# Optimization experiments

Measured on AMD Instinct MI355X. Metric: run time of the kernel, lower is better.

## Reference

```python
import jax, jax.numpy as jnp
import numpy as np

N, E, D, H, ED = 50000, 800000, 64, 8, 16
DH = D // H  # 8


def setup_inputs() -> dict:
    key = jax.random.key(0)
    ks = jax.random.split(key, 16)
    s = 0.05
    return {
        "x": jax.random.normal(ks[0], (N, D), jnp.float32),
        "edge_index": jax.random.randint(ks[1], (2, E), 0, N, jnp.int32),
        "edge_attr": jax.random.normal(ks[2], (E, ED), jnp.float32),
        "Wq": jax.random.normal(ks[3], (D, D), jnp.float32) * s,
        "bq": jnp.zeros((D,), jnp.float32),
        "Wk": jax.random.normal(ks[4], (D, D), jnp.float32) * s,
        "bk": jnp.zeros((D,), jnp.float32),
        "Wv": jax.random.normal(ks[5], (D, D), jnp.float32) * s,
        "bv": jnp.zeros((D,), jnp.float32),
        "We": jax.random.normal(ks[6], (ED, D), jnp.float32) * s,
        "be": jnp.zeros((D,), jnp.float32),
        "Wskip": jax.random.normal(ks[7], (D, D), jnp.float32) * s,
        "bskip": jnp.zeros((D,), jnp.float32),
        "Wbeta": jax.random.normal(ks[8], (3 * D, 1), jnp.float32) * s,
        "gamma": jnp.ones((D,), jnp.float32),
        "beta_bn": jnp.zeros((D,), jnp.float32),
    }


def reference(x, edge_index, edge_attr, Wq, bq, Wk, bk, Wv, bv, We, be,
              Wskip, bskip, Wbeta, gamma, beta_bn):
    n, d = x.shape
    src, dst = edge_index[0], edge_index[1]
    # per-node projections, then gather per edge (PyG TransformerConv)
    q = (x @ Wq + bq).reshape(n, H, DH)
    k = (x @ Wk + bk).reshape(n, H, DH)
    v = (x @ Wv + bv).reshape(n, H, DH)
    e = (edge_attr @ We + be).reshape(-1, H, DH)
    ke = k[src] + e                      # [E,H,DH]
    ve = v[src] + e                      # [E,H,DH]
    logits = (q[dst] * ke).sum(-1) / jnp.sqrt(jnp.float32(DH))  # [E,H]
    # segment softmax over incoming edges of each destination node
    m = jax.ops.segment_max(logits, dst, num_segments=n)
    p = jnp.exp(logits - m[dst])
    denom = jax.ops.segment_sum(p, dst, num_segments=n)
    alpha = p / (denom[dst] + 1e-16)     # [E,H]
    out = jax.ops.segment_sum(alpha[:, :, None] * ve, dst, num_segments=n)
    out = out.reshape(n, d)              # concat heads
    # beta-gated skip connection (beta=True, root_weight=True)
    x_r = x @ Wskip + bskip
    g = jax.nn.sigmoid(jnp.concatenate([out, x_r, out - x_r], axis=-1) @ Wbeta)
    out = g * x_r + (1.0 - g) * out
    # BatchNorm1d (training forward: batch statistics), eps=1e-5
    mean = out.mean(axis=0)
    var = out.var(axis=0)
    out = (out - mean) * jax.lax.rsqrt(var + 1e-5) * gamma + beta_bn
    # LeakyReLU(0.01); dropout is identity in eval
    return jnp.where(out >= 0, out, 0.01 * out)
```

## Files before the change

kernel.cpp:

```cpp
#include <hip/hip_runtime.h>

#define D   64
#define H   8
#define DH  8
#define ED  16
#define QK_SCALE 0.35355339059327373f

typedef unsigned int uint_t;

__device__ __forceinline__ void fma4(float4& a, float s, const float4& w) {
    a.x += s * w.x; a.y += s * w.y; a.z += s * w.z; a.w += s * w.w;
}
__device__ __forceinline__ uint_t f2bf(float f) {
    uint_t u = __float_as_uint(f);
    return (u + 0x7FFFu + ((u >> 16) & 1u)) >> 16;
}
__device__ __forceinline__ float bf_lo(uint_t u) { return __uint_as_float(u << 16); }
__device__ __forceinline__ float bf_hi(uint_t u) { return __uint_as_float(u & 0xFFFF0000u); }

__global__ __launch_bounds__(256) void proj_qs_hist(
    const float* __restrict__ x,
    const float* __restrict__ Wq, const float* __restrict__ bq,
    const float* __restrict__ Ws, const float* __restrict__ bs,
    const float* __restrict__ We, const float* __restrict__ be,
    float* __restrict__ q, float* __restrict__ xr,
    uint_t* __restrict__ Ap, float* __restrict__ qbe, int N,
    const int* __restrict__ ei, int* __restrict__ cnt, int E, int projBlocks)
{
    __shared__ float sW[2][D * D];
    __shared__ float sWe[ED * D];
    __shared__ float sbe[D];
    if (blockIdx.x >= projBlocks) {
        int gid = (blockIdx.x - projBlocks) * 256 + threadIdx.x;
        if (gid < E) atomicAdd(&cnt[ei[E + gid]], 1);
        return;
    }
    {
        for (int t = threadIdx.x; t < D * D; t += 256) {
            sW[0][t] = Wq[t];
            sW[1][t] = Ws[t];
        }
        for (int t = threadIdx.x; t < ED * D; t += 256) sWe[t] = We[t];
        if (threadIdx.x < D) sbe[threadIdx.x] = be[threadIdx.x];
    }
    __syncthreads();

    int cg = (threadIdx.x & 15) * 4;
    float4 vbq = *(const float4*)(bq + cg);
    float4 vbs = *(const float4*)(bs + cg);
    int h  = cg >> 3;
    int hh = (cg >> 2) & 1;

    #pragma unroll 1
    for (int it = 0; it < 4; ++it) {
        int node = blockIdx.x * 64 + it * 16 + (threadIdx.x >> 4);
        if (node >= N) return;

        float4 aq = {0,0,0,0}, as_ = {0,0,0,0};
        const float* xrow = x + (size_t)node * D;

        #pragma unroll
        for (int i = 0; i < D; i += 4) {
            float4 xv = *(const float4*)(xrow + i);
            #pragma unroll
            for (int s = 0; s < 4; ++s) {
                float xs = (&xv.x)[s];
                fma4(aq,  xs, *(const float4*)(&sW[0][(i + s) * D + cg]));
                fma4(as_, xs, *(const float4*)(&sW[1][(i + s) * D + cg]));
            }
        }
        aq.x = (aq.x + vbq.x) * QK_SCALE;
        aq.y = (aq.y + vbq.y) * QK_SCALE;
        aq.z = (aq.z + vbq.z) * QK_SCALE;
        aq.w = (aq.w + vbq.w) * QK_SCALE;
        as_.x += vbs.x; as_.y += vbs.y; as_.z += vbs.z; as_.w += vbs.w;

        size_t o = (size_t)node * D + cg;
        *(float4*)(q  + o) = aq;
        *(float4*)(xr + o) = as_;

        float part[ED];
        #pragma unroll
        for (int i = 0; i < ED; ++i) {
            float pi = 0.f;
            #pragma unroll
            for (int s = 0; s < 4; ++s)
                pi += (&aq.x)[s] * sWe[i * D + cg + s];
            part[i] = pi;
        }
        float qb = 0.f;
        #pragma unroll
        for (int s = 0; s < 4; ++s) qb += (&aq.x)[s] * sbe[cg + s];
        #pragma unroll
        for (int i = 0; i < ED; ++i) part[i] += __shfl_xor(part[i], 1);
        qb += __shfl_xor(qb, 1);

        uint4 apk;
        apk.x = f2bf(part[hh * 8 + 0]) | (f2bf(part[hh * 8 + 1]) << 16);
        apk.y = f2bf(part[hh * 8 + 2]) | (f2bf(part[hh * 8 + 3]) << 16);
        apk.z = f2bf(part[hh * 8 + 4]) | (f2bf(part[hh * 8 + 5]) << 16);
        apk.w = f2bf(part[hh * 8 + 6]) | (f2bf(part[hh * 8 + 7]) << 16);
        *(uint4*)(Ap + (size_t)node * 64 + h * 8 + hh * 4) = apk;
        if (hh == 0) qbe[(size_t)node * 8 + h] = qb;
    }
}

__global__ __launch_bounds__(256) void proj_kv_scana(
    const float* __restrict__ x,
    const float* __restrict__ Wk, const float* __restrict__ bk,
    const float* __restrict__ Wv, const float* __restrict__ bv,
    uint_t* __restrict__ kvp, int N, int kvBlocks,
    const int* __restrict__ cnt, int* __restrict__ bsum)
{
    __shared__ float sW[2][D * D];
    __shared__ int red[256];
    if (blockIdx.x >= kvBlocks) {
        int t = threadIdx.x;
        int i = (blockIdx.x - kvBlocks) * 256 + t;
        red[t] = (i < N) ? cnt[i] : 0;
        __syncthreads();
        for (int s = 128; s > 0; s >>= 1) {
            if (t < s) red[t] += red[t + s];
            __syncthreads();
        }
        if (t == 0) bsum[blockIdx.x - kvBlocks] = red[0];
        return;
    }
    for (int t = threadIdx.x; t < D * D; t += 256) {
        sW[0][t] = Wk[t];
        sW[1][t] = Wv[t];
    }
    __syncthreads();

    int cg = (threadIdx.x & 15) * 4;
    float4 vbk = *(const float4*)(bk + cg);
    float4 vbv = *(const float4*)(bv + cg);

    #pragma unroll 1
    for (int it = 0; it < 4; ++it) {
        int node = blockIdx.x * 64 + it * 16 + (threadIdx.x >> 4);
        if (node >= N) return;

        float4 ak = {0,0,0,0}, av = {0,0,0,0};
        const float* xrow = x + (size_t)node * D;

        #pragma unroll
        for (int i = 0; i < D; i += 4) {
            float4 xv = *(const float4*)(xrow + i);
            #pragma unroll
            for (int s = 0; s < 4; ++s) {
                float xs = (&xv.x)[s];
                fma4(ak, xs, *(const float4*)(&sW[0][(i + s) * D + cg]));
                fma4(av, xs, *(const float4*)(&sW[1][(i + s) * D + cg]));
            }
        }
        ak.x += vbk.x; ak.y += vbk.y; ak.z += vbk.z; ak.w += vbk.w;
        av.x += vbv.x; av.y += vbv.y; av.z += vbv.z; av.w += vbv.w;

        uint4 pkv;
        pkv.x = f2bf(ak.x) | (f2bf(av.x) << 16);
        pkv.y = f2bf(ak.y) | (f2bf(av.y) << 16);
        pkv.z = f2bf(ak.z) | (f2bf(av.z) << 16);
        pkv.w = f2bf(ak.w) | (f2bf(av.w) << 16);
        *(uint4*)(kvp + (size_t)node * D + cg) = pkv;
    }
}

__global__ __launch_bounds__(256) void scan_b(int* __restrict__ bsum, int nb)
{
    __shared__ int sh[256];
    int t = threadIdx.x;
    int v = (t < nb) ? bsum[t] : 0;
    sh[t] = v;
    __syncthreads();
    for (int s = 1; s < 256; s <<= 1) {
        int a = (t >= s) ? sh[t - s] : 0;
        __syncthreads();
        sh[t] += a;
        __syncthreads();
    }
    if (t < nb) bsum[t] = sh[t] - v;
}

__global__ __launch_bounds__(256) void scan_c(
    const int* __restrict__ cnt, const int* __restrict__ bsum,
    int* __restrict__ row_start, int* __restrict__ cursor, int N, int E)
{
    __shared__ int sh[256];
    int t = threadIdx.x;
    int i = blockIdx.x * 256 + t;
    int v = (i < N) ? cnt[i] : 0;
    sh[t] = v;
    __syncthreads();
    for (int s = 1; s < 256; s <<= 1) {
        int a = (t >= s) ? sh[t - s] : 0;
        __syncthreads();
        sh[t] += a;
        __syncthreads();
    }
    int excl = sh[t] - v + bsum[blockIdx.x];
    if (i < N) { row_start[i] = excl; cursor[i] = excl; }
    if (i == N - 1) row_start[N] = E;
}

__global__ __launch_bounds__(256) void csr_scatter(
    const int* __restrict__ ei, const float4* __restrict__ ea4,
    int* __restrict__ cursor, int* __restrict__ srcs_s,
    uint_t* __restrict__ ea_s, int E)
{
    int gid = blockIdx.x * 256 + threadIdx.x;
    if (gid >= E) return;
    int src = ei[gid];
    int dst = ei[E + gid];
    float4 r0 = ea4[(size_t)gid * 4 + 0];
    float4 r1 = ea4[(size_t)gid * 4 + 1];
    float4 r2 = ea4[(size_t)gid * 4 + 2];
    float4 r3 = ea4[(size_t)gid * 4 + 3];
    int pos = atomicAdd(&cursor[dst], 1);
    srcs_s[pos] = src;
    uint4 p0, p1;
    p0.x = f2bf(r0.x) | (f2bf(r0.y) << 16);
    p0.y = f2bf(r0.z) | (f2bf(r0.w) << 16);
    p0.z = f2bf(r1.x) | (f2bf(r1.y) << 16);
    p0.w = f2bf(r1.z) | (f2bf(r1.w) << 16);
    p1.x = f2bf(r2.x) | (f2bf(r2.y) << 16);
    p1.y = f2bf(r2.z) | (f2bf(r2.w) << 16);
    p1.z = f2bf(r3.x) | (f2bf(r3.y) << 16);
    p1.w = f2bf(r3.z) | (f2bf(r3.w) << 16);
    *(uint4*)(ea_s + (size_t)pos * 8)     = p0;
    *(uint4*)(ea_s + (size_t)pos * 8 + 4) = p1;
}

__global__ __launch_bounds__(256, 4) void node_gather(
    const int*   __restrict__ row_start,
    const int*   __restrict__ srcs_s,
    const uint_t* __restrict__ ea_s,
    const float* __restrict__ We, const float* __restrict__ be,
    const float* __restrict__ q, const uint_t* __restrict__ kvp,
    const float* __restrict__ xr,
    const uint_t* __restrict__ Ap, const float* __restrict__ qbe,
    const float* __restrict__ Wbeta,
    float* __restrict__ out, float* __restrict__ S1p, float* __restrict__ S2p,
    int N)
{
    __shared__ float l1[4][D];
    __shared__ float l2[4][D];
    int lane = threadIdx.x & 63;
    int w    = threadIdx.x >> 6;
    int h    = lane & 7;
    int e    = lane >> 3;
    int cmix = h * 8 + e;
    int perm = (h << 3) | e;

    float rWe[ED];
    #pragma unroll
    for (int i = 0; i < ED; ++i) rWe[i] = We[i * D + cmix];
    float bev = be[cmix];
    float wb0 = Wbeta[lane], wb1 = Wbeta[D + lane], wb2 = Wbeta[2 * D + lane];

    float s1bn = 0.f, s2bn = 0.f;
    int stride = gridDim.x * 4;

    for (int nid = blockIdx.x * 4 + w; nid < N; nid += stride) {
        int rs  = row_start[nid];
        int deg = row_start[nid + 1] - rs;

        const float* qp = q + (size_t)nid * D + h * 8;
        float4 q0 = *(const float4*)qp;
        float4 q1 = *(const float4*)(qp + 4);
        const uint4* app = (const uint4*)(Ap + (size_t)nid * 64 + h * 8);
        uint4 au0 = app[0], au1 = app[1];
        float a16[ED];
        #pragma unroll
        for (int j = 0; j < 4; ++j) {
            a16[(j & 3) * 2]     = bf_lo((&au0.x)[j]);
            a16[(j & 3) * 2 + 1] = bf_hi((&au0.x)[j]);
            a16[8 + (j & 3) * 2]     = bf_lo((&au1.x)[j]);
            a16[8 + (j & 3) * 2 + 1] = bf_hi((&au1.x)[j]);
        }
        float qbeh = qbe[(size_t)nid * 8 + h];

        float acc[8] = {0,0,0,0,0,0,0,0};
        float sv[ED] = {0,0,0,0,0,0,0,0,0,0,0,0,0,0,0,0};
        float den = 0.f;

        for (int j0 = 0; j0 < deg; j0 += 8) {
            int eidx = j0 + e;
            bool valid = eidx < deg;
            int ce = valid ? eidx : 0;
            int src = srcs_s[rs + ce];

            const uint4* kp = (const uint4*)(kvp + (size_t)src * 64 + h * 8);
            uint4 k0 = kp[0], k1 = kp[1];
            const uint4* ep = (const uint4*)(ea_s + (size_t)(rs + ce) * 8);
            uint4 e0 = ep[0], e1 = ep[1];

            float ex[ED];
            #pragma unroll
            for (int j = 0; j < 4; ++j) {
                ex[j * 2]         = bf_lo((&e0.x)[j]);
                ex[j * 2 + 1]     = bf_hi((&e0.x)[j]);
                ex[8 + j * 2]     = bf_lo((&e1.x)[j]);
                ex[8 + j * 2 + 1] = bf_hi((&e1.x)[j]);
            }
            float c = qbeh;
            c += (&q0.x)[0] * bf_lo(k0.x); c += (&q0.x)[1] * bf_lo(k0.y);
            c += (&q0.x)[2] * bf_lo(k0.z); c += (&q0.x)[3] * bf_lo(k0.w);
            c += (&q1.x)[0] * bf_lo(k1.x); c += (&q1.x)[1] * bf_lo(k1.y);
            c += (&q1.x)[2] * bf_lo(k1.z); c += (&q1.x)[3] * bf_lo(k1.w);
            #pragma unroll
            for (int i = 0; i < ED; ++i) c += ex[i] * a16[i];

            float p = valid ? __expf(c) : 0.f;
            den += p;
            acc[0] += p * bf_hi(k0.x); acc[1] += p * bf_hi(k0.y);
            acc[2] += p * bf_hi(k0.z); acc[3] += p * bf_hi(k0.w);
            acc[4] += p * bf_hi(k1.x); acc[5] += p * bf_hi(k1.y);
            acc[6] += p * bf_hi(k1.z); acc[7] += p * bf_hi(k1.w);
            #pragma unroll
            for (int i = 0; i < ED; ++i) sv[i] += p * ex[i];
        }

        #pragma unroll
        for (int m = 8; m <= 32; m <<= 1) {
            den += __shfl_xor(den, m);
            #pragma unroll
            for (int i = 0; i < 8; ++i) acc[i] += __shfl_xor(acc[i], m);
            #pragma unroll
            for (int i = 0; i < ED; ++i) sv[i] += __shfl_xor(sv[i], m);
        }
        float vsum = acc[0];
        #pragma unroll
        for (int i = 1; i < 8; ++i) vsum = (e == i) ? acc[i] : vsum;
        float esum = 0.f;
        #pragma unroll
        for (int i = 0; i < ED; ++i) esum += rWe[i] * sv[i];

        float o_mix = (vsum + esum + bev * den) / (den + 1e-16f);
        float o = __shfl(o_mix, perm);

        float xrv = xr[(size_t)nid * D + lane];
        float tb  = o * wb0 + xrv * wb1 + (o - xrv) * wb2;
        #pragma unroll
        for (int s = 1; s < 64; s <<= 1) tb += __shfl_xor(tb, s);
        float g  = 1.f / (1.f + __expf(-tb));
        float o2 = g * xrv + (1.f - g) * o;
        out[(size_t)nid * D + lane] = o2;
        s1bn += o2; s2bn += o2 * o2;
    }

    l1[w][lane] = s1bn; l2[w][lane] = s2bn;
    __syncthreads();
    if (threadIdx.x < D) {
        float a = l1[0][threadIdx.x] + l1[1][threadIdx.x]
                + l1[2][threadIdx.x] + l1[3][threadIdx.x];
        float b = l2[0][threadIdx.x] + l2[1][threadIdx.x]
                + l2[2][threadIdx.x] + l2[3][threadIdx.x];
        unsafeAtomicAdd(&S1p[threadIdx.x * 64], a);
        unsafeAtomicAdd(&S2p[threadIdx.x * 64], b);
    }
}

__global__ __launch_bounds__(256) void bn_apply(
    float4* __restrict__ out, const float* __restrict__ S1p,
    const float* __restrict__ S2p, const float* __restrict__ gamma,
    const float* __restrict__ beta, int total4, float invN)
{
    int gid = blockIdx.x * 256 + threadIdx.x;
    if (gid >= total4) return;
    int col = (gid & 15) * 4;
    float4 g4 = *(const float4*)(gamma + col);
    float4 b4 = *(const float4*)(beta + col);
    float4 y  = out[gid];
    #pragma unroll
    for (int j = 0; j < 4; ++j) {
        float mean = S1p[(col + j) * 64] * invN;
        float var  = S2p[(col + j) * 64] * invN - mean * mean;
        float sc   = (&g4.x)[j] * rsqrtf(var + 1e-5f);
        float sh   = (&b4.x)[j] - mean * sc;
        float tv   = (&y.x)[j] * sc + sh;
        (&y.x)[j]  = (tv >= 0.f) ? tv : 0.01f * tv;
    }
    out[gid] = y;
}

extern "C" void kernel_launch(void* const* d_in, const int* in_sizes, int n_in,
                              void* d_out, int out_size, void* d_ws, size_t ws_size,
                              hipStream_t stream)
{
    const float* x     = (const float*)d_in[0];
    const int*   ei    = (const int*)  d_in[1];
    const float* ea    = (const float*)d_in[2];
    const float* Wq    = (const float*)d_in[3];
    const float* bq    = (const float*)d_in[4];
    const float* Wk    = (const float*)d_in[5];
    const float* bk    = (const float*)d_in[6];
    const float* Wv    = (const float*)d_in[7];
    const float* bv    = (const float*)d_in[8];
    const float* We    = (const float*)d_in[9];
    const float* be    = (const float*)d_in[10];
    const float* Wskip = (const float*)d_in[11];
    const float* bskip = (const float*)d_in[12];
    const float* Wbeta = (const float*)d_in[13];
    const float* gamma = (const float*)d_in[14];
    const float* betab = (const float*)d_in[15];

    int N = in_sizes[0] / D;
    int E = in_sizes[1] / 2;

    int*    ws        = (int*)d_ws;
    int*    cnt       = ws;
    float*  S1p       = (float*)(ws + 50000);
    float*  S2p       = (float*)(ws + 54096);
    int*    row_start = ws + 58192;
    int*    bsum      = ws + 108240;
    int*    srcs_s    = ws + 108544;
    uint_t* ea_s      = (uint_t*)(ws + 908544);
    uint_t* kvp       = (uint_t*)(ws + 7308544);
    float*  q         = (float*)(ws + 10508544);
    float*  xr        = (float*)(ws + 13708544);
    uint_t* Ap        = (uint_t*)(ws + 16908544);
    float*  qbe       = (float*)(ws + 20108544);

    hipMemsetAsync(d_ws, 0, (size_t)58192 * sizeof(int), stream);

    int projB = (N + 63) / 64;
    int histB = (E + 255) / 256;
    proj_qs_hist<<<projB + histB, 256, 0, stream>>>(
        x, Wq, bq, Wskip, bskip, We, be,
        q, xr, Ap, qbe, N, ei, cnt, E, projB);

    int scanB = (N + 255) / 256;
    proj_kv_scana<<<projB + scanB, 256, 0, stream>>>(
        x, Wk, bk, Wv, bv, kvp, N, projB, cnt, bsum);

    scan_b<<<1, 256, 0, stream>>>(bsum, scanB);
    scan_c<<<scanB, 256, 0, stream>>>(cnt, bsum, row_start, cnt, N, E);

    csr_scatter<<<(E + 255) / 256, 256, 0, stream>>>(
        ei, (const float4*)ea, cnt, srcs_s, ea_s, E);

    node_gather<<<1024, 256, 0, stream>>>(
        row_start, srcs_s, ea_s, We, be, q, kvp, xr, Ap, qbe, Wbeta,
        (float*)d_out, S1p, S2p, N);

    bn_apply<<<(N * 16 + 255) / 256, 256, 0, stream>>>(
        (float4*)d_out, S1p, S2p, gamma, betab, N * 16, 1.0f / (float)N);
}
```

Before: 217.6 us.

## Fuse block-sum scan into scan_c, prefetch edge sources, cheaper head-sum reduce

Removes the separate single-block scan_b launch: each scan_c block now redundantly scans the block sums in shared memory to find its own offset. In node_gather, the next iteration's source index is prefetched so the dependent kvp gather is issued earlier. The 8-element accumulator butterfly is replaced by a halving transpose-reduce (7 shuffles instead of 24), and lanes are remapped so the final output permutation shuffle disappears. This costs a little redundant scan work per block and changes which lane writes which output column.

```diff
diff --git a/kernel.cpp b/kernel.cpp
--- a/kernel.cpp
+++ b/kernel.cpp
@@ -17,6 +17,27 @@
 }
 __device__ __forceinline__ float bf_lo(uint_t u) { return __uint_as_float(u << 16); }
 __device__ __forceinline__ float bf_hi(uint_t u) { return __uint_as_float(u & 0xFFFF0000u); }
+
+__device__ __forceinline__ float khreduce8(const float* acc, int e) {
+    int b0 = e & 1, b1 = (e >> 1) & 1, b2 = (e >> 2) & 1;
+    float t0[4];
+    #pragma unroll
+    for (int j = 0; j < 4; ++j) {
+        float k = b0 ? acc[2*j+1] : acc[2*j];
+        float s = b0 ? acc[2*j]   : acc[2*j+1];
+        t0[j] = k + __shfl_xor(s, 8);
+    }
+    float t1[2];
+    #pragma unroll
+    for (int j = 0; j < 2; ++j) {
+        float k = b1 ? t0[2*j+1] : t0[2*j];
+        float s = b1 ? t0[2*j]   : t0[2*j+1];
+        t1[j] = k + __shfl_xor(s, 16);
+    }
+    float k = b2 ? t1[1] : t1[0];
+    float s = b2 ? t1[0] : t1[1];
+    return k + __shfl_xor(s, 32);
+}
 
 __global__ __launch_bounds__(256) void proj_qs_hist(
     const float* __restrict__ x,
@@ -166,28 +187,24 @@
     }
 }
 
-__global__ __launch_bounds__(256) void scan_b(int* __restrict__ bsum, int nb)
-{
+__global__ __launch_bounds__(256) void scan_c(
+    const int* __restrict__ cnt, const int* __restrict__ bsum,
+    int* __restrict__ row_start, int* __restrict__ cursor, int N, int E, int nb)
+{
+    __shared__ int sb[256];
     __shared__ int sh[256];
     int t = threadIdx.x;
-    int v = (t < nb) ? bsum[t] : 0;
-    sh[t] = v;
+    int bv = (t < nb) ? bsum[t] : 0;
+    sb[t] = bv;
     __syncthreads();
     for (int s = 1; s < 256; s <<= 1) {
-        int a = (t >= s) ? sh[t - s] : 0;
+        int a = (t >= s) ? sb[t - s] : 0;
         __syncthreads();
-        sh[t] += a;
+        sb[t] += a;
         __syncthreads();
     }
-    if (t < nb) bsum[t] = sh[t] - v;
-}
-
-__global__ __launch_bounds__(256) void scan_c(
-    const int* __restrict__ cnt, const int* __restrict__ bsum,
-    int* __restrict__ row_start, int* __restrict__ cursor, int N, int E)
-{
-    __shared__ int sh[256];
-    int t = threadIdx.x;
+    int boff = sb[blockIdx.x] - bsum[blockIdx.x];
+
     int i = blockIdx.x * 256 + t;
     int v = (i < N) ? cnt[i] : 0;
     sh[t] = v;
@@ -198,7 +215,7 @@
         sh[t] += a;
         __syncthreads();
     }
-    int excl = sh[t] - v + bsum[blockIdx.x];
+    int excl = sh[t] - v + boff;
     if (i < N) { row_start[i] = excl; cursor[i] = excl; }
     if (i == N - 1) row_start[N] = E;
 }
@@ -250,13 +267,12 @@
     int h    = lane & 7;
     int e    = lane >> 3;
     int cmix = h * 8 + e;
-    int perm = (h << 3) | e;
 
     float rWe[ED];
     #pragma unroll
     for (int i = 0; i < ED; ++i) rWe[i] = We[i * D + cmix];
     float bev = be[cmix];
-    float wb0 = Wbeta[lane], wb1 = Wbeta[D + lane], wb2 = Wbeta[2 * D + lane];
+    float wb0 = Wbeta[cmix], wb1 = Wbeta[D + cmix], wb2 = Wbeta[2 * D + cmix];
 
     float s1bn = 0.f, s2bn = 0.f;
     int stride = gridDim.x * 4;
@@ -273,10 +289,10 @@
         float a16[ED];
         #pragma unroll
         for (int j = 0; j < 4; ++j) {
-            a16[(j & 3) * 2]     = bf_lo((&au0.x)[j]);
-            a16[(j & 3) * 2 + 1] = bf_hi((&au0.x)[j]);
-            a16[8 + (j & 3) * 2]     = bf_lo((&au1.x)[j]);
-            a16[8 + (j & 3) * 2 + 1] = bf_hi((&au1.x)[j]);
+            a16[j * 2]         = bf_lo((&au0.x)[j]);
+            a16[j * 2 + 1]     = bf_hi((&au0.x)[j]);
+            a16[8 + j * 2]     = bf_lo((&au1.x)[j]);
+            a16[8 + j * 2 + 1] = bf_hi((&au1.x)[j]);
         }
         float qbeh = qbe[(size_t)nid * 8 + h];
 
@@ -284,24 +300,30 @@
         float sv[ED] = {0,0,0,0,0,0,0,0,0,0,0,0,0,0,0,0};
         float den = 0.f;
 
+        int src_next = (e < deg) ? srcs_s[rs + e] : 0;
+
         for (int j0 = 0; j0 < deg; j0 += 8) {
+            int src = src_next;
+            {
+                int enx = j0 + 8 + e;
+                src_next = (enx < deg) ? srcs_s[rs + enx] : 0;
+            }
             int eidx = j0 + e;
             bool valid = eidx < deg;
             int ce = valid ? eidx : 0;
-            int src = srcs_s[rs + ce];
 
             const uint4* kp = (const uint4*)(kvp + (size_t)src * 64 + h * 8);
             uint4 k0 = kp[0], k1 = kp[1];
             const uint4* ep = (const uint4*)(ea_s + (size_t)(rs + ce) * 8);
-            uint4 e0 = ep[0], e1 = ep[1];
+            uint4 u0 = ep[0], u1 = ep[1];
 
             float ex[ED];
             #pragma unroll
             for (int j = 0; j < 4; ++j) {
-                ex[j * 2]         = bf_lo((&e0.x)[j]);
-                ex[j * 2 + 1]     = bf_hi((&e0.x)[j]);
-                ex[8 + j * 2]     = bf_lo((&e1.x)[j]);
-                ex[8 + j * 2 + 1] = bf_hi((&e1.x)[j]);
+                ex[j * 2]         = bf_lo((&u0.x)[j]);
+                ex[j * 2 + 1]     = bf_hi((&u0.x)[j]);
+                ex[8 + j * 2]     = bf_lo((&u1.x)[j]);
+                ex[8 + j * 2 + 1] = bf_hi((&u1.x)[j]);
             }
             float c = qbeh;
             c += (&q0.x)[0] * bf_lo(k0.x); c += (&q0.x)[1] * bf_lo(k0.y);
@@ -325,31 +347,27 @@
         for (int m = 8; m <= 32; m <<= 1) {
             den += __shfl_xor(den, m);
             #pragma unroll
-            for (int i = 0; i < 8; ++i) acc[i] += __shfl_xor(acc[i], m);
-            #pragma unroll
             for (int i = 0; i < ED; ++i) sv[i] += __shfl_xor(sv[i], m);
         }
-        float vsum = acc[0];
-        #pragma unroll
-        for (int i = 1; i < 8; ++i) vsum = (e == i) ? acc[i] : vsum;
+        float vsum = khreduce8(acc, e);
+
         float esum = 0.f;
         #pragma unroll
         for (int i = 0; i < ED; ++i) esum += rWe[i] * sv[i];
 
-        float o_mix = (vsum + esum + bev * den) / (den + 1e-16f);
-        float o = __shfl(o_mix, perm);
-
-        float xrv = xr[(size_t)nid * D + lane];
+        float o = (vsum + esum + bev * den) / (den + 1e-16f);
+
+        float xrv = xr[(size_t)nid * D + cmix];
         float tb  = o * wb0 + xrv * wb1 + (o - xrv) * wb2;
         #pragma unroll
         for (int s = 1; s < 64; s <<= 1) tb += __shfl_xor(tb, s);
         float g  = 1.f / (1.f + __expf(-tb));
         float o2 = g * xrv + (1.f - g) * o;
-        out[(size_t)nid * D + lane] = o2;
+        out[(size_t)nid * D + cmix] = o2;
         s1bn += o2; s2bn += o2 * o2;
     }
 
-    l1[w][lane] = s1bn; l2[w][lane] = s2bn;
+    l1[w][cmix] = s1bn; l2[w][cmix] = s2bn;
     __syncthreads();
     if (threadIdx.x < D) {
         float a = l1[0][threadIdx.x] + l1[1][threadIdx.x]
@@ -434,8 +452,7 @@
     proj_kv_scana<<<projB + scanB, 256, 0, stream>>>(
         x, Wk, bk, Wv, bv, kvp, N, projB, cnt, bsum);
 
-    scan_b<<<1, 256, 0, stream>>>(bsum, scanB);
-    scan_c<<<scanB, 256, 0, stream>>>(cnt, bsum, row_start, cnt, N, E);
+    scan_c<<<scanB, 256, 0, stream>>>(cnt, bsum, row_start, cnt, N, E, scanB);
 
     csr_scatter<<<(E + 255) / 256, 256, 0, stream>>>(
         ei, (const float4*)ea, cnt, srcs_s, ea_s, E);
```

Measured after the change: 208.0 us. 4.4% less time.
